# Optimization experiments

Measured on AMD Instinct MI355X. Metric: run time of the kernel, lower is better.

Reference implementation:

```python
import jax, jax.numpy as jnp
import numpy as np

LN_EPS = 1e-5
LEAKY_SLOPE = 0.01


def layer_norm(x, g, b):
    mu = jnp.mean(x, axis=-1, keepdims=True)
    var = jnp.mean(jnp.square(x - mu), axis=-1, keepdims=True)
    return (x - mu) * jax.lax.rsqrt(var + LN_EPS) * g + b


def setup_inputs() -> dict:
    key = jax.random.key(0)
    ks = jax.random.split(key, 7)
    bs, n, d = 64, 128, 64
    return {
        "embeddings": jax.random.normal(ks[0], (bs, n, d), dtype=jnp.float32),
        "ln_g": 1.0 + 0.1 * jax.random.normal(ks[1], (d,), dtype=jnp.float32),
        "ln_b": 0.1 * jax.random.normal(ks[2], (d,), dtype=jnp.float32),
        "W1": jax.random.normal(ks[3], (3 * d, d), dtype=jnp.float32) / np.sqrt(3 * d),
        "b1": 0.1 * jax.random.normal(ks[4], (d,), dtype=jnp.float32),
        "W2": jax.random.normal(ks[5], (d, 1), dtype=jnp.float32) / np.sqrt(d),
        "b2": 0.1 * jax.random.normal(ks[6], (1,), dtype=jnp.float32),
    }


def reference(embeddings, ln_g, ln_b, W1, b1, W2, b2):
    # embeddings: [bs, n, d]
    bs, n, d = embeddings.shape
    # LayerNorm of single items computed once (em_i_norm / em_j_norm are
    # just broadcast copies of this along different axes).
    xn = layer_norm(embeddings, ln_g, ln_b)  # [bs, n, d]
    # Pairwise product em_ij[b, p, q] = x[b, q] * x[b, p]
    em_ij = embeddings[:, :, None, :] * embeddings[:, None, :, :]  # [bs,n,n,d]
    em_ij_norm = layer_norm(em_ij, ln_g, ln_b)
    # Split concat-Linear into three blocks: cat order (em_i, em_j, em_ij)
    # em_i_norm[b,p,q] = xn[b,q], em_j_norm[b,p,q] = xn[b,p]
    a_i = xn @ W1[:d]          # [bs, n, d] -> broadcast over p (axis 1)
    a_j = xn @ W1[d:2 * d]     # [bs, n, d] -> broadcast over q (axis 2)
    a_ij = jnp.einsum('bpqk,kd->bpqd', em_ij_norm, W1[2 * d:])
    att_em = jnp.tanh(a_i[:, None, :, :] + a_j[:, :, None, :] + a_ij + b1)
    scores = (att_em @ W2)[..., 0] + b2[0]  # [bs, n, n]
    alphas = jax.nn.softmax(scores, axis=-1)
    ctx = jax.nn.leaky_relu(alphas[..., None] * em_ij, negative_slope=LEAKY_SLOPE)
    return jnp.sum(ctx, axis=2)  # [bs, n, d]
```

## Files before the change

kernel.cpp:

```cpp
#include <hip/hip_runtime.h>
#include <hip/hip_bf16.h>

#define LN_EPS 1e-5f
#define S2LE 2.885390081777927f
#define L2E  1.4426950408889634f
#define XST 68

typedef __attribute__((ext_vector_type(8))) short bf16x8;
typedef __attribute__((ext_vector_type(4))) float f32x4;

__device__ __forceinline__ float wsum(float v) {
    #pragma unroll
    for (int off = 32; off; off >>= 1) v += __shfl_xor(v, off, 64);
    return v;
}
__device__ __forceinline__ float wmax(float v) {
    #pragma unroll
    for (int off = 32; off; off >>= 1) v = fmaxf(v, __shfl_xor(v, off, 64));
    return v;
}
__device__ __forceinline__ bf16x8 pack8(float4 a, float4 b) {
    __hip_bfloat162 h0 = __float22bfloat162_rn(float2{a.x, a.y});
    __hip_bfloat162 h1 = __float22bfloat162_rn(float2{a.z, a.w});
    __hip_bfloat162 h2 = __float22bfloat162_rn(float2{b.x, b.y});
    __hip_bfloat162 h3 = __float22bfloat162_rn(float2{b.z, b.w});
    short2 s0 = *reinterpret_cast<short2*>(&h0);
    short2 s1 = *reinterpret_cast<short2*>(&h1);
    short2 s2 = *reinterpret_cast<short2*>(&h2);
    short2 s3 = *reinterpret_cast<short2*>(&h3);
    bf16x8 r;
    r[0] = s0.x; r[1] = s0.y; r[2] = s1.x; r[3] = s1.y;
    r[4] = s2.x; r[5] = s2.y; r[6] = s3.x; r[7] = s3.y;
    return r;
}
__device__ __forceinline__ float fexp2(float x) {
#if __has_builtin(__builtin_amdgcn_exp2f)
    return __builtin_amdgcn_exp2f(x);
#else
    return exp2f(x);
#endif
}
__device__ __forceinline__ float frcp(float x) {
#if __has_builtin(__builtin_amdgcn_rcpf)
    return __builtin_amdgcn_rcpf(x);
#else
    return 1.f / x;
#endif
}

__global__ __launch_bounds__(256) void att1_prep(
    const float* __restrict__ emb, const float* __restrict__ g,
    const float* __restrict__ bln, const float* __restrict__ W1,
    const float* __restrict__ b1, const float* __restrict__ W2,
    const float* __restrict__ b2, float* __restrict__ ai,
    float* __restrict__ aj, short* __restrict__ afrag,
    float* __restrict__ Tf, float* __restrict__ Sx,
    float* __restrict__ c2, float* __restrict__ consts)
{
    const int bid = blockIdx.x, tid = threadIdx.x, lane = tid & 63, wid = tid >> 6;
    if (bid < 512) {
        __shared__ float w_s[8192];
        __shared__ float xn_s[4][64];
        for (int i = tid * 4; i < 8192; i += 1024)
            *(float4*)&w_s[i] = *(const float4*)&W1[i];
        __syncthreads();
        #pragma unroll
        for (int it = 0; it < 4; ++it) {
            const int r = bid * 16 + it * 4 + wid;
            float x = emb[r * 64 + lane];
            float m = wsum(x) * (1.f / 64.f);
            float xc = x - m;
            float var = wsum(xc * xc) * (1.f / 64.f);
            float xn = xc * rsqrtf(var + LN_EPS) * g[lane] + bln[lane];
            xn_s[wid][lane] = xn;
            float a0 = 0.f, a1 = 0.f;
            #pragma unroll
            for (int k = 0; k < 64; ++k) {
                float xnk = xn_s[wid][k];
                a0 = fmaf(xnk, w_s[k * 64 + lane], a0);
                a1 = fmaf(xnk, w_s[(64 + k) * 64 + lane], a1);
            }
            ai[r * 64 + lane] = a0 * S2LE;
            aj[r * 64 + lane] = a1 * S2LE;
        }
    } else if (bid < 768) {
        const int id = (bid - 512) * 4 + wid;
        const int h = id & 1, qt = (id >> 1) & 7, bb = id >> 4;
        const int q = 16 * qt + (lane & 15);
        const int k = 32 * h + 8 * (lane >> 4);
        const float* src = emb + (bb * 128 + q) * 64 + k;
        float4 v0 = ((const float4*)src)[0];
        float4 v1 = ((const float4*)src)[1];
        *(bf16x8*)(afrag + (size_t)(id * 64 + lane) * 8) = pack8(v0, v1);
    } else {
        for (int slot = tid; slot < 512; slot += 256) {
            int l = slot & 63, h = (slot >> 6) & 1, dt = slot >> 7;
            int n = 4 * (l & 15) + dt;
            int k = 32 * h + 8 * (l >> 4);
            #pragma unroll
            for (int j = 0; j < 8; ++j)
                Tf[slot * 8 + j] = g[k + j] * W1[(128 + k + j) * 64 + n];
        }
        if (tid < 64) {
            float S = 0.f, c = 0.f;
            for (int k = 0; k < 64; ++k) {
                float w = W1[(128 + k) * 64 + tid];
                S = fmaf(g[k], w, S);
                c = fmaf(bln[k], w, c);
            }
            Sx[tid] = S;
            c2[tid] = (c + b1[tid]) * S2LE;
            if (tid == 0) {
                float sw = 0.f;
                for (int d = 0; d < 64; ++d) sw += W2[d];
                consts[0] = sw + b2[0];
            }
        }
    }
}

__global__ __launch_bounds__(512) void att1_main(
    const float* __restrict__ emb, const short* __restrict__ afrag,
    const float* __restrict__ Tf, const float* __restrict__ Sx,
    const float* __restrict__ c2a, const float* __restrict__ W2,
    const float* __restrict__ consts, const float* __restrict__ ai,
    const float* __restrict__ aj, float* __restrict__ out)
{
    __shared__ float xb_s[128 * XST];
    __shared__ float muWS[8][128];
    __shared__ float rsWS[8][128];
    __shared__ float scWS[8][128];

    const int tid = threadIdx.x, lane = tid & 63, w = tid >> 6;
    const int b = blockIdx.y;
    const int p = blockIdx.x * 8 + w;
    const int bp = b * 128 + p;
    const float* embB = emb + b * 8192;

    {
        const int r0 = tid >> 4, c0 = (tid & 15) * 4;
        #pragma unroll
        for (int pass = 0; pass < 4; ++pass) {
            int r = r0 + pass * 32;
            *(float4*)&xb_s[r * XST + c0] = *(const float4*)&embB[r * 64 + c0];
        }
    }
    __syncthreads();

    const int g4 = lane >> 4, dl = lane & 15;
    const int d0 = 4 * dl;

    float4 S4f = *(const float4*)(Sx + d0);
    float4 c2f = *(const float4*)(c2a + d0);
    float4 w2f = *(const float4*)(W2 + d0);
    float S4[4]   = {S4f.x, S4f.y, S4f.z, S4f.w};
    float w2m2[4] = {-2.f * w2f.x, -2.f * w2f.y, -2.f * w2f.z, -2.f * w2f.w};
    const float sw2b2 = consts[0];
    float4 ajf = *(const float4*)(aj + (size_t)bp * 64 + d0);
    float ajc[4] = {ajf.x + c2f.x, ajf.y + c2f.y, ajf.z + c2f.z, ajf.w + c2f.w};

    bf16x8 bfr[4][2];
    #pragma unroll
    for (int h = 0; h < 2; ++h) {
        const float* xr = &xb_s[p * XST + 32 * h + 8 * g4];
        float4 x0 = *(const float4*)xr, x1 = *(const float4*)(xr + 4);
        #pragma unroll
        for (int dt = 0; dt < 4; ++dt) {
            const float4* tf = (const float4*)(Tf + (size_t)((dt * 2 + h) * 64 + lane) * 8);
            float4 t0 = tf[0], t1 = tf[1];
            float4 u0 = {t0.x * x0.x, t0.y * x0.y, t0.z * x0.z, t0.w * x0.w};
            float4 u1 = {t1.x * x1.x, t1.y * x1.y, t1.z * x1.z, t1.w * x1.w};
            bfr[dt][h] = pack8(u0, u1);
        }
    }

    {
        const float* xpr = &xb_s[p * XST];
        const float* xqa = &xb_s[lane * XST];
        const float* xqb = &xb_s[(64 + lane) * XST];
        float sa = 0.f, sa2 = 0.f, sb = 0.f, sb2 = 0.f;
        #pragma unroll
        for (int j = 0; j < 16; ++j) {
            float4 a = *(const float4*)(xpr + 4 * j);
            float4 qa = *(const float4*)(xqa + 4 * j);
            float4 qb = *(const float4*)(xqb + 4 * j);
            float a0 = a.x * qa.x, a1 = a.y * qa.y, a2 = a.z * qa.z, a3 = a.w * qa.w;
            sa += a0 + a1 + a2 + a3;
            sa2 = fmaf(a0, a0, fmaf(a1, a1, fmaf(a2, a2, fmaf(a3, a3, sa2))));
            float b0 = a.x * qb.x, b1v = a.y * qb.y, b2v = a.z * qb.z, b3 = a.w * qb.w;
            sb += b0 + b1v + b2v + b3;
            sb2 = fmaf(b0, b0, fmaf(b1v, b1v, fmaf(b2v, b2v, fmaf(b3, b3, sb2))));
        }
        float ma = sa * (1.f / 64.f);
        float va = fmaxf(sa2 * (1.f / 64.f) - ma * ma, 0.f);
        muWS[w][lane] = ma;
        rsWS[w][lane] = rsqrtf(va + LN_EPS) * S2LE;
        float mb = sb * (1.f / 64.f);
        float vb = fmaxf(sb2 * (1.f / 64.f) - mb * mb, 0.f);
        muWS[w][64 + lane] = mb;
        rsWS[w][64 + lane] = rsqrtf(vb + LN_EPS) * S2LE;
    }

    #pragma unroll 2
    for (int qt = 0; qt < 8; ++qt) {
        bf16x8 afr0 = *(const bf16x8*)(afrag + (size_t)((b * 16 + 2 * qt + 0) * 64 + lane) * 8);
        bf16x8 afr1 = *(const bf16x8*)(afrag + (size_t)((b * 16 + 2 * qt + 1) * 64 + lane) * 8);
        f32x4 acc[4];
        #pragma unroll
        for (int dt = 0; dt < 4; ++dt) {
            f32x4 c = {0.f, 0.f, 0.f, 0.f};
            c = __builtin_amdgcn_mfma_f32_16x16x32_bf16(afr0, bfr[dt][0], c, 0, 0, 0);
            c = __builtin_amdgcn_mfma_f32_16x16x32_bf16(afr1, bfr[dt][1], c, 0, 0, 0);
            acc[dt] = c;
        }

        const int q0 = 16 * qt + 4 * g4;
        float4 mu4 = *(const float4*)&muWS[w][q0];
        float4 rs4 = *(const float4*)&rsWS[w][q0];
        float muA[4] = {mu4.x, mu4.y, mu4.z, mu4.w};
        float rsA[4] = {rs4.x, rs4.y, rs4.z, rs4.w};

        const float* aibase = ai + (size_t)(b * 128 + q0) * 64 + d0;
        float part[4];
        #pragma unroll
        for (int r = 0; r < 4; ++r) {
            float4 aif = *(const float4*)(aibase + r * 64);
            float aiv[4] = {aif.x, aif.y, aif.z, aif.w};
            float rmu = rsA[r] * muA[r];
            float pr = 0.f;
            #pragma unroll
            for (int dt = 0; dt < 4; ++dt) {
                float xv = fmaf(rsA[r], acc[dt][r], fmaf(-rmu, S4[dt], ajc[dt]) + aiv[dt]);
                float e = fexp2(xv);
                pr = fmaf(w2m2[dt], frcp(e + 1.f), pr);
            }
            part[r] = pr;
        }
        #pragma unroll
        for (int r = 0; r < 4; ++r) {
            #pragma unroll
            for (int off = 1; off <= 8; off <<= 1)
                part[r] += __shfl_xor(part[r], off, 64);
        }
        if (dl == 0) {
            float4 sc = {part[0] + sw2b2, part[1] + sw2b2, part[2] + sw2b2, part[3] + sw2b2};
            *(float4*)&scWS[w][q0] = sc;
        }
    }

    {
        float s0 = scWS[w][lane], s1 = scWS[w][64 + lane];
        float M = wmax(fmaxf(s0, s1));
        float e0 = fexp2((s0 - M) * L2E), e1 = fexp2((s1 - M) * L2E);
        float rZ = frcp(wsum(e0 + e1));
        scWS[w][lane] = e0 * rZ;
        scWS[w][64 + lane] = e1 * rZ;
    }

    {
        float4 S1 = {0.f, 0.f, 0.f, 0.f}, S2 = {0.f, 0.f, 0.f, 0.f};
        #pragma unroll 8
        for (int i = 0; i < 32; ++i) {
            int q = 4 * i + g4;
            float al = scWS[w][q];
            float4 xq = *(const float4*)&xb_s[q * XST + d0];
            S1.x = fmaf(al, xq.x, S1.x); S1.y = fmaf(al, xq.y, S1.y);
            S1.z = fmaf(al, xq.z, S1.z); S1.w = fmaf(al, xq.w, S1.w);
            S2.x = fmaf(al, fabsf(xq.x), S2.x); S2.y = fmaf(al, fabsf(xq.y), S2.y);
            S2.z = fmaf(al, fabsf(xq.z), S2.z); S2.w = fmaf(al, fabsf(xq.w), S2.w);
        }
        #pragma unroll
        for (int off = 16; off <= 32; off <<= 1) {
            S1.x += __shfl_xor(S1.x, off, 64); S1.y += __shfl_xor(S1.y, off, 64);
            S1.z += __shfl_xor(S1.z, off, 64); S1.w += __shfl_xor(S1.w, off, 64);
            S2.x += __shfl_xor(S2.x, off, 64); S2.y += __shfl_xor(S2.y, off, 64);
            S2.z += __shfl_xor(S2.z, off, 64); S2.w += __shfl_xor(S2.w, off, 64);
        }
        if (g4 == 0) {
            float4 xp4 = *(const float4*)&xb_s[p * XST + d0];
            float4 o;
            o.x = fmaf(0.505f * xp4.x, S1.x, 0.495f * fabsf(xp4.x) * S2.x);
            o.y = fmaf(0.505f * xp4.y, S1.y, 0.495f * fabsf(xp4.y) * S2.y);
            o.z = fmaf(0.505f * xp4.z, S1.z, 0.495f * fabsf(xp4.z) * S2.z);
            o.w = fmaf(0.505f * xp4.w, S1.w, 0.495f * fabsf(xp4.w) * S2.w);
            *(float4*)&out[(size_t)bp * 64 + d0] = o;
        }
    }
}

extern "C" void kernel_launch(void* const* d_in, const int* in_sizes, int n_in,
                              void* d_out, int out_size, void* d_ws, size_t ws_size,
                              hipStream_t stream) {
    const float* emb = (const float*)d_in[0];
    const float* g   = (const float*)d_in[1];
    const float* bln = (const float*)d_in[2];
    const float* W1  = (const float*)d_in[3];
    const float* b1  = (const float*)d_in[4];
    const float* W2  = (const float*)d_in[5];
    const float* b2  = (const float*)d_in[6];
    float* out = (float*)d_out;

    float* ws = (float*)d_ws;
    float* ai = ws;
    float* aj = ws + 524288;
    float* Tf = ws + 1048576;
    float* Sx = ws + 1052672;
    float* c2 = ws + 1052736;
    float* consts = ws + 1052800;
    short* af = (short*)(ws + 1052864);

    att1_prep<<<769, 256, 0, stream>>>(emb, g, bln, W1, b1, W2, b2,
                                       ai, aj, af, Tf, Sx, c2, consts);
    att1_main<<<dim3(16, 64), 512, 0, stream>>>(emb, af, Tf, Sx, c2, W2, consts,
                                                ai, aj, out);
}
```

Measured before the change: 59.34 us.

## Transpose MFMA output so each lane holds one q, shrink blocks to four waves

Swaps the MFMA operand order and reorders the Tf weight layout so that each accumulator lane holds a single q row across 16 d values. Per-q LayerNorm stats now stay in registers and are broadcast by shuffle, which removes the shared-memory mu/rs arrays and reduces the per-qt reduction to two shuffles. Blocks shrink from 8 waves to 4 (grid 32x64, launch_bounds 256,4) to raise occupancy. The cost is more per-lane register arrays (16-wide S/aj/w2), and each block now reloads the full 128-row embedding tile for only 4 rows of p.

```diff
diff --git a/kernel.cpp b/kernel.cpp
--- a/kernel.cpp
+++ b/kernel.cpp
@@ -95,7 +95,7 @@
     } else {
         for (int slot = tid; slot < 512; slot += 256) {
             int l = slot & 63, h = (slot >> 6) & 1, dt = slot >> 7;
-            int n = 4 * (l & 15) + dt;
+            int n = 16 * dt + (l & 15);
             int k = 32 * h + 8 * (l >> 4);
             #pragma unroll
             for (int j = 0; j < 8; ++j)
@@ -119,7 +119,7 @@
     }
 }
 
-__global__ __launch_bounds__(512) void att1_main(
+__global__ __launch_bounds__(256, 4) void att1_main(
     const float* __restrict__ emb, const short* __restrict__ afrag,
     const float* __restrict__ Tf, const float* __restrict__ Sx,
     const float* __restrict__ c2a, const float* __restrict__ W2,
@@ -127,37 +127,41 @@
     const float* __restrict__ aj, float* __restrict__ out)
 {
     __shared__ float xb_s[128 * XST];
-    __shared__ float muWS[8][128];
-    __shared__ float rsWS[8][128];
-    __shared__ float scWS[8][128];
+    __shared__ float scWS[4][128];
 
     const int tid = threadIdx.x, lane = tid & 63, w = tid >> 6;
     const int b = blockIdx.y;
-    const int p = blockIdx.x * 8 + w;
+    const int p = blockIdx.x * 4 + w;
     const int bp = b * 128 + p;
     const float* embB = emb + b * 8192;
 
     {
         const int r0 = tid >> 4, c0 = (tid & 15) * 4;
         #pragma unroll
-        for (int pass = 0; pass < 4; ++pass) {
-            int r = r0 + pass * 32;
+        for (int pass = 0; pass < 8; ++pass) {
+            int r = r0 + pass * 16;
             *(float4*)&xb_s[r * XST + c0] = *(const float4*)&embB[r * 64 + c0];
         }
     }
     __syncthreads();
 
     const int g4 = lane >> 4, dl = lane & 15;
-    const int d0 = 4 * dl;
-
-    float4 S4f = *(const float4*)(Sx + d0);
-    float4 c2f = *(const float4*)(c2a + d0);
-    float4 w2f = *(const float4*)(W2 + d0);
-    float S4[4]   = {S4f.x, S4f.y, S4f.z, S4f.w};
-    float w2m2[4] = {-2.f * w2f.x, -2.f * w2f.y, -2.f * w2f.z, -2.f * w2f.w};
+
+    float S4a[16], ajca[16], w2a[16];
+    #pragma unroll
+    for (int dt = 0; dt < 4; ++dt) {
+        const int db = 16 * dt + 4 * g4;
+        float4 sv = *(const float4*)(Sx + db);
+        float4 cv = *(const float4*)(c2a + db);
+        float4 av = *(const float4*)(aj + (size_t)bp * 64 + db);
+        float4 wv = *(const float4*)(W2 + db);
+        S4a[dt*4+0] = sv.x; S4a[dt*4+1] = sv.y; S4a[dt*4+2] = sv.z; S4a[dt*4+3] = sv.w;
+        ajca[dt*4+0] = av.x + cv.x; ajca[dt*4+1] = av.y + cv.y;
+        ajca[dt*4+2] = av.z + cv.z; ajca[dt*4+3] = av.w + cv.w;
+        w2a[dt*4+0] = -2.f * wv.x; w2a[dt*4+1] = -2.f * wv.y;
+        w2a[dt*4+2] = -2.f * wv.z; w2a[dt*4+3] = -2.f * wv.w;
+    }
     const float sw2b2 = consts[0];
-    float4 ajf = *(const float4*)(aj + (size_t)bp * 64 + d0);
-    float ajc[4] = {ajf.x + c2f.x, ajf.y + c2f.y, ajf.z + c2f.z, ajf.w + c2f.w};
 
     bf16x8 bfr[4][2];
     #pragma unroll
@@ -174,6 +178,7 @@
         }
     }
 
+    float ma, rsa, mb, rsb;
     {
         const float* xpr = &xb_s[p * XST];
         const float* xqa = &xb_s[lane * XST];
@@ -191,15 +196,15 @@
             sb += b0 + b1v + b2v + b3;
             sb2 = fmaf(b0, b0, fmaf(b1v, b1v, fmaf(b2v, b2v, fmaf(b3, b3, sb2))));
         }
-        float ma = sa * (1.f / 64.f);
+        ma = sa * (1.f / 64.f);
         float va = fmaxf(sa2 * (1.f / 64.f) - ma * ma, 0.f);
-        muWS[w][lane] = ma;
-        rsWS[w][lane] = rsqrtf(va + LN_EPS) * S2LE;
-        float mb = sb * (1.f / 64.f);
+        rsa = rsqrtf(va + LN_EPS) * S2LE;
+        mb = sb * (1.f / 64.f);
         float vb = fmaxf(sb2 * (1.f / 64.f) - mb * mb, 0.f);
-        muWS[w][64 + lane] = mb;
-        rsWS[w][64 + lane] = rsqrtf(vb + LN_EPS) * S2LE;
-    }
+        rsb = rsqrtf(vb + LN_EPS) * S2LE;
+    }
+
+    const float* ai_ln = ai + ((size_t)(b * 128) + dl) * 64 + 4 * g4;
 
     #pragma unroll 2
     for (int qt = 0; qt < 8; ++qt) {
@@ -209,43 +214,35 @@
         #pragma unroll
         for (int dt = 0; dt < 4; ++dt) {
             f32x4 c = {0.f, 0.f, 0.f, 0.f};
-            c = __builtin_amdgcn_mfma_f32_16x16x32_bf16(afr0, bfr[dt][0], c, 0, 0, 0);
-            c = __builtin_amdgcn_mfma_f32_16x16x32_bf16(afr1, bfr[dt][1], c, 0, 0, 0);
+            c = __builtin_amdgcn_mfma_f32_16x16x32_bf16(bfr[dt][0], afr0, c, 0, 0, 0);
+            c = __builtin_amdgcn_mfma_f32_16x16x32_bf16(bfr[dt][1], afr1, c, 0, 0, 0);
             acc[dt] = c;
         }
 
-        const int q0 = 16 * qt + 4 * g4;
-        float4 mu4 = *(const float4*)&muWS[w][q0];
-        float4 rs4 = *(const float4*)&rsWS[w][q0];
-        float muA[4] = {mu4.x, mu4.y, mu4.z, mu4.w};
-        float rsA[4] = {rs4.x, rs4.y, rs4.z, rs4.w};
-
-        const float* aibase = ai + (size_t)(b * 128 + q0) * 64 + d0;
-        float part[4];
-        #pragma unroll
-        for (int r = 0; r < 4; ++r) {
-            float4 aif = *(const float4*)(aibase + r * 64);
+        float msel = (qt < 4) ? ma : mb;
+        float rsel = (qt < 4) ? rsa : rsb;
+        const int srcl = (16 * qt + dl) & 63;
+        float muv = __shfl(msel, srcl, 64);
+        float rsv = __shfl(rsel, srcl, 64);
+        float rmu = rsv * muv;
+
+        const float* aiq = ai_ln + (size_t)qt * 1024;
+        float pr = 0.f;
+        #pragma unroll
+        for (int dt = 0; dt < 4; ++dt) {
+            float4 aif = *(const float4*)(aiq + dt * 16);
             float aiv[4] = {aif.x, aif.y, aif.z, aif.w};
-            float rmu = rsA[r] * muA[r];
-            float pr = 0.f;
             #pragma unroll
-            for (int dt = 0; dt < 4; ++dt) {
-                float xv = fmaf(rsA[r], acc[dt][r], fmaf(-rmu, S4[dt], ajc[dt]) + aiv[dt]);
+            for (int r = 0; r < 4; ++r) {
+                float t = ajca[dt * 4 + r] + aiv[r];
+                float xv = fmaf(rsv, acc[dt][r], fmaf(-rmu, S4a[dt * 4 + r], t));
                 float e = fexp2(xv);
-                pr = fmaf(w2m2[dt], frcp(e + 1.f), pr);
+                pr = fmaf(w2a[dt * 4 + r], frcp(e + 1.f), pr);
             }
-            part[r] = pr;
-        }
-        #pragma unroll
-        for (int r = 0; r < 4; ++r) {
-            #pragma unroll
-            for (int off = 1; off <= 8; off <<= 1)
-                part[r] += __shfl_xor(part[r], off, 64);
-        }
-        if (dl == 0) {
-            float4 sc = {part[0] + sw2b2, part[1] + sw2b2, part[2] + sw2b2, part[3] + sw2b2};
-            *(float4*)&scWS[w][q0] = sc;
-        }
+        }
+        pr += __shfl_xor(pr, 16, 64);
+        pr += __shfl_xor(pr, 32, 64);
+        if (lane < 16) scWS[w][16 * qt + lane] = pr + sw2b2;
     }
 
     {
@@ -258,6 +255,7 @@
     }
 
     {
+        const int d0 = 4 * dl;
         float4 S1 = {0.f, 0.f, 0.f, 0.f}, S2 = {0.f, 0.f, 0.f, 0.f};
         #pragma unroll 8
         for (int i = 0; i < 32; ++i) {
@@ -311,6 +309,6 @@
 
     att1_prep<<<769, 256, 0, stream>>>(emb, g, bln, W1, b1, W2, b2,
                                        ai, aj, af, Tf, Sx, c2, consts);
-    att1_main<<<dim3(16, 64), 512, 0, stream>>>(emb, af, Tf, Sx, c2, W2, consts,
+    att1_main<<<dim3(32, 64), 256, 0, stream>>>(emb, af, Tf, Sx, c2, W2, consts,
                                                 ai, aj, out);
 }
```

New measurement: 74.36 us. 25.3% more time.
